# Kernel tuning notes

Hardware: AMD Instinct MI355X
Metric: run time of the kernel (lower is better)

## Reference

```python
import jax, jax.numpy as jnp
import numpy as np

N_NODES = 50000
N_EDGES = 800000
NODE_IN, EDGE_IN, EFT, OUT = 128, 64, 32, 64


def setup_inputs() -> dict:
    key = jax.random.key(0)
    ks = jax.random.split(key, 8)
    h = jax.random.normal(ks[0], (N_NODES, NODE_IN), dtype=jnp.float32)
    edge_feat = jax.random.normal(ks[1], (N_EDGES, EDGE_IN), dtype=jnp.float32)
    src = jax.random.randint(ks[2], (N_EDGES,), 0, N_NODES, dtype=jnp.int32)
    dst = jax.random.randint(ks[3], (N_EDGES,), 0, N_NODES, dtype=jnp.int32)
    Wn = jax.random.normal(ks[4], (OUT, NODE_IN), dtype=jnp.float32) * 0.05
    We = jax.random.normal(ks[5], (EFT, EDGE_IN), dtype=jnp.float32) * 0.05
    Wa = jax.random.normal(ks[6], (1, OUT + EFT + OUT), dtype=jnp.float32) * 0.05
    W2 = jax.random.normal(ks[7], (OUT, OUT + EFT), dtype=jnp.float32) * 0.05
    return {"h": h, "edge_feat": edge_feat, "src": src, "dst": dst,
            "Wn": Wn, "We": We, "Wa": Wa, "W2": W2}


def reference(h, edge_feat, src, dst, Wn, We, Wa, W2):
    N = h.shape[0]
    # node / edge feature projections (bias=False linears)
    z = h @ Wn.T                       # [N, OUT]
    ef = edge_feat @ We.T              # [E, EFT]
    # per-edge message: concat(src node ft, edge ft)
    zne = jnp.concatenate([z[src], ef], axis=1)            # [E, OUT+EFT]
    # attention logit: leaky_relu(attn_fc([zne, z_dst]))
    a = jnp.concatenate([zne, z[dst]], axis=1) @ Wa.T      # [E, 1]
    s = jax.nn.leaky_relu(a[:, 0], negative_slope=0.01)    # [E]
    # segment softmax over incoming edges of each dst node
    seg_max = jax.ops.segment_max(s, dst, num_segments=N)
    ex = jnp.exp(s - seg_max[dst])
    denom = jax.ops.segment_sum(ex, dst, num_segments=N)
    alpha = ex / denom[dst]                                # [E]
    # weighted scatter-sum aggregation, then fc2
    agg = jax.ops.segment_sum(alpha[:, None] * zne, dst, num_segments=N)
    h_new = agg @ W2.T                                     # [N, OUT]
    # DGL semantics: nodes with no incoming messages keep ndata['z'] = fc_n(h)
    deg = jax.ops.segment_sum(jnp.ones_like(s), dst, num_segments=N)
    return jnp.where((deg > 0)[:, None], h_new, z)
```

## Files before the change

kernel.cpp:

```cpp
#include <hip/hip_runtime.h>
#include <math.h>

#define N_NODES 50000
#define N_EDGES 800000
#define NB1 196

typedef __attribute__((ext_vector_type(8))) short bf16x8;
typedef __attribute__((ext_vector_type(4))) float f32x4;

__device__ __forceinline__ unsigned short f2bf(float f) {
    unsigned u = __float_as_uint(f);
    unsigned r = (u + 0x7FFFu + ((u >> 16) & 1u)) >> 16;
    return (unsigned short)r;
}
__device__ __forceinline__ float bf2f(unsigned short u) {
    return __uint_as_float(((unsigned)u) << 16);
}
__device__ __forceinline__ unsigned pack2bf(float a, float b) {
    return (unsigned)f2bf(a) | ((unsigned)f2bf(b) << 16);
}

__global__ __launch_bounds__(256) void kw_kernel(const float* __restrict__ We,
                                                 const float* __restrict__ Wa,
                                                 const float* __restrict__ Wn,
                                                 const float* __restrict__ W2,
                                                 short* __restrict__ Bpack,
                                                 int* __restrict__ degi) {
    int t = blockIdx.x * 256 + threadIdx.x;
    if (t < N_NODES) degi[t] = 0;
    if (t < 15360) {
        int f = t >> 9, u = t & 511, lane = u >> 3, j = u & 7;
        int c = lane & 15, G = lane >> 4;
        float v = 0.f;
        if (f < 4) {
            int s = f >> 1, n = f & 1;
            v = We[(16 * n + c) * 64 + 32 * s + 8 * G + j];
        } else if (f < 6) {
            int s = f - 4;
            if (c == 0) {
                int k = 32 * s + 8 * G + j;
                #pragma unroll
                for (int jj = 0; jj < 32; ++jj) v += Wa[64 + jj] * We[jj * 64 + k];
            }
        } else if (f < 22) {
            int qf = f - 6, s = qf >> 2, n = qf & 3;
            v = Wn[(16 * n + c) * 128 + 32 * s + 8 * G + j];
        } else {
            int qf = f - 22, s = qf >> 2, n = qf & 3;
            v = W2[(16 * n + c) * 96 + 32 * s + 8 * G + j];
        }
        Bpack[t] = (short)f2bf(v);
    }
}

__global__ __launch_bounds__(256) void node_hist_kernel(
    const float* __restrict__ h, const float* __restrict__ Wa,
    const short* __restrict__ Bpack, const int* __restrict__ dst,
    float* __restrict__ z, unsigned short* __restrict__ y16,
    float* __restrict__ asrc, float* __restrict__ adst,
    int* __restrict__ degi, int* __restrict__ ranks)
{
    __shared__ float zl[4][1088];
    int t = threadIdx.x;
    if (blockIdx.x >= 782) {
        int e = (blockIdx.x - 782) * 256 + t;
        if (e < N_EDGES) ranks[e] = atomicAdd(&degi[dst[e]], 1);
        return;
    }
    int w = t >> 6, l = t & 63, c = l & 15, G = l >> 4;
    int T = blockIdx.x * 4 + w;
    if (T >= 3125) return;
    int n0 = T * 16;
    const bf16x8* Bp = (const bf16x8*)Bpack;

    const float* hp = h + (size_t)(n0 + c) * 128 + 8 * G;
    bf16x8 a[4];
    #pragma unroll
    for (int s = 0; s < 4; ++s) {
        float4 lo = *(const float4*)(hp + 32 * s);
        float4 hi = *(const float4*)(hp + 32 * s + 4);
        a[s][0] = (short)f2bf(lo.x); a[s][1] = (short)f2bf(lo.y);
        a[s][2] = (short)f2bf(lo.z); a[s][3] = (short)f2bf(lo.w);
        a[s][4] = (short)f2bf(hi.x); a[s][5] = (short)f2bf(hi.y);
        a[s][6] = (short)f2bf(hi.z); a[s][7] = (short)f2bf(hi.w);
    }
    f32x4 acc[4] = {{0.f,0.f,0.f,0.f},{0.f,0.f,0.f,0.f},{0.f,0.f,0.f,0.f},{0.f,0.f,0.f,0.f}};
    #pragma unroll
    for (int n = 0; n < 4; ++n)
        #pragma unroll
        for (int s = 0; s < 4; ++s)
            acc[n] = __builtin_amdgcn_mfma_f32_16x16x32_bf16(a[s], Bp[(6 + 4*s + n)*64 + l], acc[n], 0, 0, 0);

    float was[4], wad[4];
    #pragma unroll
    for (int n = 0; n < 4; ++n) { was[n] = Wa[16*n + c]; wad[n] = Wa[96 + 16*n + c]; }

    #pragma unroll
    for (int r = 0; r < 4; ++r) {
        int row = n0 + 4 * G + r;
        #pragma unroll
        for (int n = 0; n < 4; ++n) {
            z[(size_t)row * 64 + 16 * n + c] = acc[n][r];
            zl[w][(4 * G + r) * 68 + 16 * n + c] = acc[n][r];
        }
        float ps = acc[0][r]*was[0] + acc[1][r]*was[1] + acc[2][r]*was[2] + acc[3][r]*was[3];
        float pd = acc[0][r]*wad[0] + acc[1][r]*wad[1] + acc[2][r]*wad[2] + acc[3][r]*wad[3];
        ps += __shfl_xor(ps, 1); ps += __shfl_xor(ps, 2);
        ps += __shfl_xor(ps, 4); ps += __shfl_xor(ps, 8);
        pd += __shfl_xor(pd, 1); pd += __shfl_xor(pd, 2);
        pd += __shfl_xor(pd, 4); pd += __shfl_xor(pd, 8);
        if (c == 0) { asrc[row] = ps; adst[row] = pd; }
    }

    bf16x8 ay[2];
    #pragma unroll
    for (int s = 0; s < 2; ++s)
        #pragma unroll
        for (int j = 0; j < 8; ++j)
            ay[s][j] = (short)f2bf(zl[w][c * 68 + 32 * s + 8 * G + j]);
    f32x4 accy[4] = {{0.f,0.f,0.f,0.f},{0.f,0.f,0.f,0.f},{0.f,0.f,0.f,0.f},{0.f,0.f,0.f,0.f}};
    #pragma unroll
    for (int n = 0; n < 4; ++n)
        #pragma unroll
        for (int s = 0; s < 2; ++s)
            accy[n] = __builtin_amdgcn_mfma_f32_16x16x32_bf16(ay[s], Bp[(22 + 4*s + n)*64 + l], accy[n], 0, 0, 0);
    #pragma unroll
    for (int r = 0; r < 4; ++r)
        #pragma unroll
        for (int n = 0; n < 4; ++n)
            y16[(size_t)(n0 + 4*G + r) * 64 + 16*n + c] = f2bf(accy[n][r]);
}

__global__ __launch_bounds__(256) void scan1_kernel(const int* __restrict__ degi,
                                                    int* __restrict__ partial) {
    int t = threadIdx.x, i = blockIdx.x * 256 + t;
    int d = (i < N_NODES) ? degi[i] : 0;
    #pragma unroll
    for (int off = 32; off; off >>= 1) d += __shfl_down(d, off);
    __shared__ int wsum[4];
    if ((t & 63) == 0) wsum[t >> 6] = d;
    __syncthreads();
    if (t == 0) partial[blockIdx.x] = wsum[0] + wsum[1] + wsum[2] + wsum[3];
}

__global__ __launch_bounds__(256) void scan2_kernel(int* __restrict__ partial) {
    __shared__ int s[256];
    int t = threadIdx.x;
    int v = (t < NB1) ? partial[t] : 0;
    s[t] = v; __syncthreads();
    for (int off = 1; off < 256; off <<= 1) {
        int x = (t >= off) ? s[t - off] : 0;
        __syncthreads();
        s[t] += x;
        __syncthreads();
    }
    if (t < NB1) partial[t] = s[t] - v;
}

__global__ __launch_bounds__(256) void scan3_kernel(const int* __restrict__ degi,
                                                    const int* __restrict__ partial,
                                                    int* __restrict__ start) {
    __shared__ int s[256];
    int t = threadIdx.x, i = blockIdx.x * 256 + t;
    int d = (i < N_NODES) ? degi[i] : 0;
    s[t] = d; __syncthreads();
    for (int off = 1; off < 256; off <<= 1) {
        int x = (t >= off) ? s[t - off] : 0;
        __syncthreads();
        s[t] += x;
        __syncthreads();
    }
    if (i < N_NODES) start[i] = partial[blockIdx.x] + s[t] - d;
}

__global__ __launch_bounds__(256, 2) void edge_scatter_kernel(
    const float* __restrict__ edge_feat, const int* __restrict__ src,
    const int* __restrict__ dst, const float* __restrict__ asrc,
    const float* __restrict__ adst, const short* __restrict__ Bpack,
    const int* __restrict__ ranks, const int* __restrict__ start,
    unsigned* __restrict__ gout, float* __restrict__ exarr,
    int2* __restrict__ edata)
{
    int t = threadIdx.x;
    if (blockIdx.x >= 3125) {
        int e = (blockIdx.x - 3125) * 256 + t;
        if (e < N_EDGES) edata[start[dst[e]] + ranks[e]] = make_int2(e, src[e]);
        return;
    }
    int w = t >> 6, l = t & 63;
    int c = l & 15, G = l >> 4;
    int wbase = blockIdx.x * 256 + w * 64;

    const bf16x8* Bp = (const bf16x8*)Bpack;
    bf16x8 b00 = Bp[0 * 64 + l];
    bf16x8 b01 = Bp[1 * 64 + l];
    bf16x8 b10 = Bp[2 * 64 + l];
    bf16x8 b11 = Bp[3 * 64 + l];
    bf16x8 b2a = Bp[4 * 64 + l];
    bf16x8 b2b = Bp[5 * 64 + l];

    int e = wbase + l;
    float apre = asrc[src[e]] + adst[dst[e]];
    float Ra[16];
    #pragma unroll
    for (int k = 0; k < 4; ++k)
        #pragma unroll
        for (int r = 0; r < 4; ++r)
            Ra[4 * k + r] = __shfl(apre, 16 * k + 4 * G + r);

    const float* efr = edge_feat + (size_t)(wbase + c) * 64 + G * 8;
    float4 n0 = *(const float4*)(efr);
    float4 n1 = *(const float4*)(efr + 4);
    float4 n2 = *(const float4*)(efr + 32);
    float4 n3 = *(const float4*)(efr + 36);

    #pragma unroll
    for (int k = 0; k < 4; ++k) {
        float4 c0 = n0, c1 = n1, c2 = n2, c3 = n3;
        if (k < 3) {
            const float* efn = edge_feat + (size_t)(wbase + 16 * (k + 1) + c) * 64 + G * 8;
            n0 = *(const float4*)(efn);
            n1 = *(const float4*)(efn + 4);
            n2 = *(const float4*)(efn + 32);
            n3 = *(const float4*)(efn + 36);
        }
        bf16x8 a0, a1;
        a0[0] = (short)f2bf(c0.x); a0[1] = (short)f2bf(c0.y);
        a0[2] = (short)f2bf(c0.z); a0[3] = (short)f2bf(c0.w);
        a0[4] = (short)f2bf(c1.x); a0[5] = (short)f2bf(c1.y);
        a0[6] = (short)f2bf(c1.z); a0[7] = (short)f2bf(c1.w);
        a1[0] = (short)f2bf(c2.x); a1[1] = (short)f2bf(c2.y);
        a1[2] = (short)f2bf(c2.z); a1[3] = (short)f2bf(c2.w);
        a1[4] = (short)f2bf(c3.x); a1[5] = (short)f2bf(c3.y);
        a1[6] = (short)f2bf(c3.z); a1[7] = (short)f2bf(c3.w);

        f32x4 acc0 = {0.f, 0.f, 0.f, 0.f};
        f32x4 acc1 = {0.f, 0.f, 0.f, 0.f};
        f32x4 acc2 = {0.f, 0.f, 0.f, 0.f};
        acc0 = __builtin_amdgcn_mfma_f32_16x16x32_bf16(a0, b00, acc0, 0, 0, 0);
        acc0 = __builtin_amdgcn_mfma_f32_16x16x32_bf16(a1, b10, acc0, 0, 0, 0);
        acc1 = __builtin_amdgcn_mfma_f32_16x16x32_bf16(a0, b01, acc1, 0, 0, 0);
        acc1 = __builtin_amdgcn_mfma_f32_16x16x32_bf16(a1, b11, acc1, 0, 0, 0);
        acc2 = __builtin_amdgcn_mfma_f32_16x16x32_bf16(a0, b2a, acc2, 0, 0, 0);
        acc2 = __builtin_amdgcn_mfma_f32_16x16x32_bf16(a1, b2b, acc2, 0, 0, 0);

        #pragma unroll
        for (int r = 0; r < 4; ++r) {
            int eo = wbase + 16 * k + 4 * G + r;
            gout[(size_t)eo * 16 + c] = pack2bf(acc0[r], acc1[r]);
            if (c == 0) {
                float aa = Ra[4 * k + r] + acc2[r];
                float sg = aa > 0.f ? aa : 0.01f * aa;
                exarr[eo] = __expf(sg);
            }
        }
    }
}

__global__ __launch_bounds__(256) void agg_kernel(
    const unsigned* __restrict__ gout, const float* __restrict__ exarr,
    const int2* __restrict__ edata, const ushort4* __restrict__ y16v,
    const int* __restrict__ start, const int* __restrict__ degi,
    const float* __restrict__ z, const float* __restrict__ W2,
    float* __restrict__ out)
{
    __shared__ float stu[4][164];
    __shared__ float sW2b[64 * 36];
    int t = threadIdx.x, w = t >> 6, l = t & 63, g = l >> 4, q = l & 15;
    for (int idx = t; idx < 64 * 32; idx += 256)
        sW2b[(idx >> 5) * 36 + (idx & 31)] = W2[(idx >> 5) * 96 + 64 + (idx & 31)];
    __syncthreads();

    int d    = blockIdx.x * 4 + w;
    int base = __builtin_amdgcn_readfirstlane(start[d]);
    int deg  = __builtin_amdgcn_readfirstlane(degi[d]);
    float2 tg = make_float2(0.f, 0.f);
    float4 uy4 = make_float4(0.f, 0.f, 0.f, 0.f);
    float den = 0.f;

    for (int c0 = 0; c0 < deg; c0 += 64) {
        int cc = min(deg - c0, 64);
        int meid = 0, msrc = 0; float mex = 0.f;
        if (l < cc) {
            int2 md = edata[base + c0 + l];
            meid = md.x; msrc = md.y;
            mex = exarr[md.x];
        }
        for (int cI = 0; cI < cc; cI += 16) {
            int e0, e1, e2, e3, s0, s1, s2, s3;
            float x0, x1, x2, x3;
            #define PREP(P, EP, SP, XP)                                      \
                { int sl = cI + 4 * P + g; bool vv = sl < cc;               \
                  int slc = vv ? sl : 0;                                     \
                  EP = __shfl(meid, slc); SP = __shfl(msrc, slc);            \
                  float xx = __shfl(mex, slc); XP = vv ? xx : 0.f; }
            PREP(0, e0, s0, x0) PREP(1, e1, s1, x1)
            PREP(2, e2, s2, x2) PREP(3, e3, s3, x3)
            #undef PREP
            unsigned ga0 = gout[(size_t)e0 * 16 + q];
            unsigned ga1 = gout[(size_t)e1 * 16 + q];
            unsigned ga2 = gout[(size_t)e2 * 16 + q];
            unsigned ga3 = gout[(size_t)e3 * 16 + q];
            ushort4 ya0 = y16v[(size_t)s0 * 16 + q];
            ushort4 ya1 = y16v[(size_t)s1 * 16 + q];
            ushort4 ya2 = y16v[(size_t)s2 * 16 + q];
            ushort4 ya3 = y16v[(size_t)s3 * 16 + q];
            #define ACCP(XP, GA, YA)                                         \
                { tg.x += XP * bf2f((unsigned short)(GA & 0xffffu));         \
                  tg.y += XP * bf2f((unsigned short)(GA >> 16));             \
                  uy4.x += XP * bf2f(YA.x); uy4.y += XP * bf2f(YA.y);        \
                  uy4.z += XP * bf2f(YA.z); uy4.w += XP * bf2f(YA.w);        \
                  den += XP; }
            ACCP(x0, ga0, ya0) ACCP(x1, ga1, ya1)
            ACCP(x2, ga2, ya2) ACCP(x3, ga3, ya3)
            #undef ACCP
        }
    }

    tg.x += __shfl_xor(tg.x, 16); tg.x += __shfl_xor(tg.x, 32);
    tg.y += __shfl_xor(tg.y, 16); tg.y += __shfl_xor(tg.y, 32);
    uy4.x += __shfl_xor(uy4.x, 16); uy4.x += __shfl_xor(uy4.x, 32);
    uy4.y += __shfl_xor(uy4.y, 16); uy4.y += __shfl_xor(uy4.y, 32);
    uy4.z += __shfl_xor(uy4.z, 16); uy4.z += __shfl_xor(uy4.z, 32);
    uy4.w += __shfl_xor(uy4.w, 16); uy4.w += __shfl_xor(uy4.w, 32);
    den += __shfl_xor(den, 16); den += __shfl_xor(den, 32);

    if (l < 16) {
        *(float4*)&stu[w][64 + q * 4] = uy4;
        stu[w][128 + q] = tg.x;
        stu[w][144 + q] = tg.y;
    }

    if (deg > 0) {
        float r = 0.f;
        #pragma unroll
        for (int k = 0; k < 8; ++k) {
            float4 wv = *(const float4*)&sW2b[l * 36 + k * 4];
            float4 vv = *(const float4*)&stu[w][128 + k * 4];
            r += wv.x * vv.x + wv.y * vv.y + wv.z * vv.z + wv.w * vv.w;
        }
        out[(size_t)d * 64 + l] = (r + stu[w][64 + l]) / den;
    } else {
        out[(size_t)d * 64 + l] = z[(size_t)d * 64 + l];
    }
}

extern "C" void kernel_launch(void* const* d_in, const int* in_sizes, int n_in,
                              void* d_out, int out_size, void* d_ws, size_t ws_size,
                              hipStream_t stream) {
    const float* h         = (const float*)d_in[0];
    const float* edge_feat = (const float*)d_in[1];
    const int*   src       = (const int*)d_in[2];
    const int*   dst       = (const int*)d_in[3];
    const float* Wn        = (const float*)d_in[4];
    const float* We        = (const float*)d_in[5];
    const float* Wa        = (const float*)d_in[6];
    const float* W2        = (const float*)d_in[7];
    float* out = (float*)d_out;

    char* p = (char*)d_ws;
    unsigned*       gout   = (unsigned*)p;       p += (size_t)N_EDGES * 16 * 4;
    float*          z      = (float*)p;          p += (size_t)N_NODES * 64 * 4;
    unsigned short* y16    = (unsigned short*)p; p += (size_t)N_NODES * 64 * 2;
    int2*           edata  = (int2*)p;           p += (size_t)N_EDGES * 8;
    float*          exarr  = (float*)p;          p += (size_t)N_EDGES * 4;
    float*          asrc   = (float*)p;          p += (size_t)N_NODES * 4;
    float*          adst   = (float*)p;          p += (size_t)N_NODES * 4;
    int*            degi   = (int*)p;            p += (size_t)N_NODES * 4;
    int*            start  = (int*)p;            p += (size_t)N_NODES * 4;
    int*            ranks  = (int*)p;            p += (size_t)N_EDGES * 4;
    int*            partial= (int*)p;            p += (size_t)256 * 4;
    short*          Bpack  = (short*)p;          p += (size_t)15360 * 2;

    kw_kernel<<<NB1, 256, 0, stream>>>(We, Wa, Wn, W2, Bpack, degi);
    node_hist_kernel<<<782 + 3125, 256, 0, stream>>>(h, Wa, Bpack, dst, z, y16,
                                                     asrc, adst, degi, ranks);
    scan1_kernel<<<NB1, 256, 0, stream>>>(degi, partial);
    scan2_kernel<<<1, 256, 0, stream>>>(partial);
    scan3_kernel<<<NB1, 256, 0, stream>>>(degi, partial, start);
    edge_scatter_kernel<<<3125 + 3125, 256, 0, stream>>>(edge_feat, src, dst, asrc, adst,
                                                         Bpack, ranks, start,
                                                         gout, exarr, edata);
    agg_kernel<<<N_NODES / 4, 256, 0, stream>>>(gout, exarr, edata, (const ushort4*)y16,
                                                start, degi, z, W2, out);
}
```

Measured before the change: 178.2 us.

## Fold W2 into edge projection and scatter full messages into dst-sorted slots

Precomputes W2[:,64:96]·We as a packed 64x64 weight, so the edge kernel produces the final 64-wide W2-projected message (edge part plus gathered y of the source node) per edge. Each message goes straight into its CSR slot by destination, along with the exp logit. The aggregation kernel then only streams contiguous bf16 rows and does a weighted sum, with no indirect gathers, edata indirection or W2 epilogue. The cost is a larger per-edge intermediate (64 bf16 instead of 32) written with scattered stores, and more MFMA work per edge.

```diff
diff --git a/kernel.cpp b/kernel.cpp
--- a/kernel.cpp
+++ b/kernel.cpp
@@ -28,25 +28,28 @@
                                                  int* __restrict__ degi) {
     int t = blockIdx.x * 256 + threadIdx.x;
     if (t < N_NODES) degi[t] = 0;
-    if (t < 15360) {
+    if (t < 34 * 512) {
         int f = t >> 9, u = t & 511, lane = u >> 3, j = u & 7;
         int c = lane & 15, G = lane >> 4;
         float v = 0.f;
-        if (f < 4) {
-            int s = f >> 1, n = f & 1;
-            v = We[(16 * n + c) * 64 + 32 * s + 8 * G + j];
-        } else if (f < 6) {
-            int s = f - 4;
+        if (f < 8) {
+            int s = f >> 2, n = f & 3;
+            int kp = 32 * s + 8 * G + j;
+            #pragma unroll
+            for (int kk = 0; kk < 32; ++kk)
+                v += W2[(16 * n + c) * 96 + 64 + kk] * We[kk * 64 + kp];
+        } else if (f < 10) {
+            int s = f - 8;
             if (c == 0) {
-                int k = 32 * s + 8 * G + j;
+                int kp = 32 * s + 8 * G + j;
                 #pragma unroll
-                for (int jj = 0; jj < 32; ++jj) v += Wa[64 + jj] * We[jj * 64 + k];
+                for (int jj = 0; jj < 32; ++jj) v += Wa[64 + jj] * We[jj * 64 + kp];
             }
-        } else if (f < 22) {
-            int qf = f - 6, s = qf >> 2, n = qf & 3;
+        } else if (f < 26) {
+            int qf = f - 10, s = qf >> 2, n = qf & 3;
             v = Wn[(16 * n + c) * 128 + 32 * s + 8 * G + j];
         } else {
-            int qf = f - 22, s = qf >> 2, n = qf & 3;
+            int qf = f - 26, s = qf >> 2, n = qf & 3;
             v = W2[(16 * n + c) * 96 + 32 * s + 8 * G + j];
         }
         Bpack[t] = (short)f2bf(v);
@@ -56,7 +59,7 @@
 __global__ __launch_bounds__(256) void node_hist_kernel(
     const float* __restrict__ h, const float* __restrict__ Wa,
     const short* __restrict__ Bpack, const int* __restrict__ dst,
-    float* __restrict__ z, unsigned short* __restrict__ y16,
+    float* __restrict__ z, ushort4* __restrict__ y16p,
     float* __restrict__ asrc, float* __restrict__ adst,
     int* __restrict__ degi, int* __restrict__ ranks)
 {
@@ -89,7 +92,7 @@
     for (int n = 0; n < 4; ++n)
         #pragma unroll
         for (int s = 0; s < 4; ++s)
-            acc[n] = __builtin_amdgcn_mfma_f32_16x16x32_bf16(a[s], Bp[(6 + 4*s + n)*64 + l], acc[n], 0, 0, 0);
+            acc[n] = __builtin_amdgcn_mfma_f32_16x16x32_bf16(a[s], Bp[(10 + 4*s + n)*64 + l], acc[n], 0, 0, 0);
 
     float was[4], wad[4];
     #pragma unroll
@@ -123,12 +126,14 @@
     for (int n = 0; n < 4; ++n)
         #pragma unroll
         for (int s = 0; s < 2; ++s)
-            accy[n] = __builtin_amdgcn_mfma_f32_16x16x32_bf16(ay[s], Bp[(22 + 4*s + n)*64 + l], accy[n], 0, 0, 0);
-    #pragma unroll
-    for (int r = 0; r < 4; ++r)
-        #pragma unroll
-        for (int n = 0; n < 4; ++n)
-            y16[(size_t)(n0 + 4*G + r) * 64 + 16*n + c] = f2bf(accy[n][r]);
+            accy[n] = __builtin_amdgcn_mfma_f32_16x16x32_bf16(ay[s], Bp[(26 + 4*s + n)*64 + l], accy[n], 0, 0, 0);
+    #pragma unroll
+    for (int r = 0; r < 4; ++r) {
+        ushort4 yo;
+        yo.x = f2bf(accy[0][r]); yo.y = f2bf(accy[1][r]);
+        yo.z = f2bf(accy[2][r]); yo.w = f2bf(accy[3][r]);
+        y16p[(size_t)(n0 + 4 * G + r) * 16 + c] = yo;
+    }
 }
 
 __global__ __launch_bounds__(256) void scan1_kernel(const int* __restrict__ degi,
@@ -173,40 +178,30 @@
     if (i < N_NODES) start[i] = partial[blockIdx.x] + s[t] - d;
 }
 
-__global__ __launch_bounds__(256, 2) void edge_scatter_kernel(
+__global__ __launch_bounds__(256, 2) void edge_kernel(
     const float* __restrict__ edge_feat, const int* __restrict__ src,
-    const int* __restrict__ dst, const float* __restrict__ asrc,
+    const int* __restrict__ dst, const int* __restrict__ ranks,
+    const int* __restrict__ start, const float* __restrict__ asrc,
     const float* __restrict__ adst, const short* __restrict__ Bpack,
-    const int* __restrict__ ranks, const int* __restrict__ start,
-    unsigned* __restrict__ gout, float* __restrict__ exarr,
-    int2* __restrict__ edata)
+    const ushort4* __restrict__ y16p,
+    unsigned short* __restrict__ wout, float* __restrict__ exslot)
 {
-    int t = threadIdx.x;
-    if (blockIdx.x >= 3125) {
-        int e = (blockIdx.x - 3125) * 256 + t;
-        if (e < N_EDGES) edata[start[dst[e]] + ranks[e]] = make_int2(e, src[e]);
-        return;
-    }
-    int w = t >> 6, l = t & 63;
+    int t = threadIdx.x, w = t >> 6, l = t & 63;
     int c = l & 15, G = l >> 4;
     int wbase = blockIdx.x * 256 + w * 64;
 
     const bf16x8* Bp = (const bf16x8*)Bpack;
-    bf16x8 b00 = Bp[0 * 64 + l];
-    bf16x8 b01 = Bp[1 * 64 + l];
-    bf16x8 b10 = Bp[2 * 64 + l];
-    bf16x8 b11 = Bp[3 * 64 + l];
-    bf16x8 b2a = Bp[4 * 64 + l];
-    bf16x8 b2b = Bp[5 * 64 + l];
+    bf16x8 bc[8];
+    #pragma unroll
+    for (int f = 0; f < 8; ++f) bc[f] = Bp[f * 64 + l];
+    bf16x8 b2a = Bp[8 * 64 + l];
+    bf16x8 b2b = Bp[9 * 64 + l];
 
     int e = wbase + l;
-    float apre = asrc[src[e]] + adst[dst[e]];
-    float Ra[16];
-    #pragma unroll
-    for (int k = 0; k < 4; ++k)
-        #pragma unroll
-        for (int r = 0; r < 4; ++r)
-            Ra[4 * k + r] = __shfl(apre, 16 * k + 4 * G + r);
+    int se = src[e];
+    int de = dst[e];
+    int slot = start[de] + ranks[e];
+    float apre = asrc[se] + adst[de];
 
     const float* efr = edge_feat + (size_t)(wbase + c) * 64 + G * 8;
     float4 n0 = *(const float4*)(efr);
@@ -224,6 +219,18 @@
             n2 = *(const float4*)(efn + 32);
             n3 = *(const float4*)(efn + 36);
         }
+        int sr[4], sl4[4]; float ap[4];
+        #pragma unroll
+        for (int r = 0; r < 4; ++r) {
+            int si = 16 * k + 4 * G + r;
+            sr[r]  = __shfl(se, si);
+            sl4[r] = __shfl(slot, si);
+            ap[r]  = __shfl(apre, si);
+        }
+        ushort4 yv[4];
+        #pragma unroll
+        for (int r = 0; r < 4; ++r) yv[r] = y16p[(size_t)sr[r] * 16 + c];
+
         bf16x8 a0, a1;
         a0[0] = (short)f2bf(c0.x); a0[1] = (short)f2bf(c0.y);
         a0[2] = (short)f2bf(c0.z); a0[3] = (short)f2bf(c0.w);
@@ -234,115 +241,66 @@
         a1[4] = (short)f2bf(c3.x); a1[5] = (short)f2bf(c3.y);
         a1[6] = (short)f2bf(c3.z); a1[7] = (short)f2bf(c3.w);
 
-        f32x4 acc0 = {0.f, 0.f, 0.f, 0.f};
-        f32x4 acc1 = {0.f, 0.f, 0.f, 0.f};
+        f32x4 acc[4] = {{0.f,0.f,0.f,0.f},{0.f,0.f,0.f,0.f},{0.f,0.f,0.f,0.f},{0.f,0.f,0.f,0.f}};
         f32x4 acc2 = {0.f, 0.f, 0.f, 0.f};
-        acc0 = __builtin_amdgcn_mfma_f32_16x16x32_bf16(a0, b00, acc0, 0, 0, 0);
-        acc0 = __builtin_amdgcn_mfma_f32_16x16x32_bf16(a1, b10, acc0, 0, 0, 0);
-        acc1 = __builtin_amdgcn_mfma_f32_16x16x32_bf16(a0, b01, acc1, 0, 0, 0);
-        acc1 = __builtin_amdgcn_mfma_f32_16x16x32_bf16(a1, b11, acc1, 0, 0, 0);
+        #pragma unroll
+        for (int n = 0; n < 4; ++n) {
+            acc[n] = __builtin_amdgcn_mfma_f32_16x16x32_bf16(a0, bc[n], acc[n], 0, 0, 0);
+            acc[n] = __builtin_amdgcn_mfma_f32_16x16x32_bf16(a1, bc[4 + n], acc[n], 0, 0, 0);
+        }
         acc2 = __builtin_amdgcn_mfma_f32_16x16x32_bf16(a0, b2a, acc2, 0, 0, 0);
         acc2 = __builtin_amdgcn_mfma_f32_16x16x32_bf16(a1, b2b, acc2, 0, 0, 0);
 
         #pragma unroll
         for (int r = 0; r < 4; ++r) {
-            int eo = wbase + 16 * k + 4 * G + r;
-            gout[(size_t)eo * 16 + c] = pack2bf(acc0[r], acc1[r]);
+            float u0 = acc[0][r] + bf2f(yv[r].x);
+            float u1 = acc[1][r] + bf2f(yv[r].y);
+            float u2 = acc[2][r] + bf2f(yv[r].z);
+            float u3 = acc[3][r] + bf2f(yv[r].w);
+            uint2 o;
+            o.x = pack2bf(u0, u1);
+            o.y = pack2bf(u2, u3);
+            *(uint2*)&wout[(size_t)sl4[r] * 64 + 4 * c] = o;
             if (c == 0) {
-                float aa = Ra[4 * k + r] + acc2[r];
+                float aa = ap[r] + acc2[r];
                 float sg = aa > 0.f ? aa : 0.01f * aa;
-                exarr[eo] = __expf(sg);
+                exslot[sl4[r]] = __expf(sg);
             }
         }
     }
 }
 
 __global__ __launch_bounds__(256) void agg_kernel(
-    const unsigned* __restrict__ gout, const float* __restrict__ exarr,
-    const int2* __restrict__ edata, const ushort4* __restrict__ y16v,
+    const unsigned short* __restrict__ wout, const float* __restrict__ exslot,
     const int* __restrict__ start, const int* __restrict__ degi,
-    const float* __restrict__ z, const float* __restrict__ W2,
-    float* __restrict__ out)
+    const float* __restrict__ z, float* __restrict__ out)
 {
-    __shared__ float stu[4][164];
-    __shared__ float sW2b[64 * 36];
-    int t = threadIdx.x, w = t >> 6, l = t & 63, g = l >> 4, q = l & 15;
-    for (int idx = t; idx < 64 * 32; idx += 256)
-        sW2b[(idx >> 5) * 36 + (idx & 31)] = W2[(idx >> 5) * 96 + 64 + (idx & 31)];
-    __syncthreads();
-
+    int t = threadIdx.x, w = t >> 6, l = t & 63;
     int d    = blockIdx.x * 4 + w;
     int base = __builtin_amdgcn_readfirstlane(start[d]);
     int deg  = __builtin_amdgcn_readfirstlane(degi[d]);
-    float2 tg = make_float2(0.f, 0.f);
-    float4 uy4 = make_float4(0.f, 0.f, 0.f, 0.f);
-    float den = 0.f;
-
-    for (int c0 = 0; c0 < deg; c0 += 64) {
-        int cc = min(deg - c0, 64);
-        int meid = 0, msrc = 0; float mex = 0.f;
-        if (l < cc) {
-            int2 md = edata[base + c0 + l];
-            meid = md.x; msrc = md.y;
-            mex = exarr[md.x];
-        }
-        for (int cI = 0; cI < cc; cI += 16) {
-            int e0, e1, e2, e3, s0, s1, s2, s3;
-            float x0, x1, x2, x3;
-            #define PREP(P, EP, SP, XP)                                      \
-                { int sl = cI + 4 * P + g; bool vv = sl < cc;               \
-                  int slc = vv ? sl : 0;                                     \
-                  EP = __shfl(meid, slc); SP = __shfl(msrc, slc);            \
-                  float xx = __shfl(mex, slc); XP = vv ? xx : 0.f; }
-            PREP(0, e0, s0, x0) PREP(1, e1, s1, x1)
-            PREP(2, e2, s2, x2) PREP(3, e3, s3, x3)
-            #undef PREP
-            unsigned ga0 = gout[(size_t)e0 * 16 + q];
-            unsigned ga1 = gout[(size_t)e1 * 16 + q];
-            unsigned ga2 = gout[(size_t)e2 * 16 + q];
-            unsigned ga3 = gout[(size_t)e3 * 16 + q];
-            ushort4 ya0 = y16v[(size_t)s0 * 16 + q];
-            ushort4 ya1 = y16v[(size_t)s1 * 16 + q];
-            ushort4 ya2 = y16v[(size_t)s2 * 16 + q];
-            ushort4 ya3 = y16v[(size_t)s3 * 16 + q];
-            #define ACCP(XP, GA, YA)                                         \
-                { tg.x += XP * bf2f((unsigned short)(GA & 0xffffu));         \
-                  tg.y += XP * bf2f((unsigned short)(GA >> 16));             \
-                  uy4.x += XP * bf2f(YA.x); uy4.y += XP * bf2f(YA.y);        \
-                  uy4.z += XP * bf2f(YA.z); uy4.w += XP * bf2f(YA.w);        \
-                  den += XP; }
-            ACCP(x0, ga0, ya0) ACCP(x1, ga1, ya1)
-            ACCP(x2, ga2, ya2) ACCP(x3, ga3, ya3)
-            #undef ACCP
-        }
-    }
-
-    tg.x += __shfl_xor(tg.x, 16); tg.x += __shfl_xor(tg.x, 32);
-    tg.y += __shfl_xor(tg.y, 16); tg.y += __shfl_xor(tg.y, 32);
-    uy4.x += __shfl_xor(uy4.x, 16); uy4.x += __shfl_xor(uy4.x, 32);
-    uy4.y += __shfl_xor(uy4.y, 16); uy4.y += __shfl_xor(uy4.y, 32);
-    uy4.z += __shfl_xor(uy4.z, 16); uy4.z += __shfl_xor(uy4.z, 32);
-    uy4.w += __shfl_xor(uy4.w, 16); uy4.w += __shfl_xor(uy4.w, 32);
-    den += __shfl_xor(den, 16); den += __shfl_xor(den, 32);
-
-    if (l < 16) {
-        *(float4*)&stu[w][64 + q * 4] = uy4;
-        stu[w][128 + q] = tg.x;
-        stu[w][144 + q] = tg.y;
-    }
-
-    if (deg > 0) {
-        float r = 0.f;
-        #pragma unroll
-        for (int k = 0; k < 8; ++k) {
-            float4 wv = *(const float4*)&sW2b[l * 36 + k * 4];
-            float4 vv = *(const float4*)&stu[w][128 + k * 4];
-            r += wv.x * vv.x + wv.y * vv.y + wv.z * vv.z + wv.w * vv.w;
-        }
-        out[(size_t)d * 64 + l] = (r + stu[w][64 + l]) / den;
-    } else {
-        out[(size_t)d * 64 + l] = z[(size_t)d * 64 + l];
-    }
+    const unsigned short* wp = wout + (size_t)base * 64 + l;
+    const float* xp = exslot + base;
+
+    float acc = 0.f, den = 0.f;
+    for (int i = 0; i < deg; i += 8) {
+        #pragma unroll
+        for (int j = 0; j < 8; ++j) {
+            int idx = i + j;
+            bool vld = idx < deg;
+            int ic = vld ? idx : deg - 1;
+            unsigned short v = wp[(size_t)ic * 64];
+            float x = vld ? xp[ic] : 0.f;
+            acc += x * bf2f(v);
+            den += x;
+        }
+    }
+
+    int comp = 16 * (l & 3) + (l >> 2);
+    if (deg > 0)
+        out[(size_t)d * 64 + comp] = acc / den;
+    else
+        out[(size_t)d * 64 + comp] = z[(size_t)d * 64 + comp];
 }
 
 extern "C" void kernel_launch(void* const* d_in, const int* in_sizes, int n_in,
@@ -359,28 +317,25 @@
     float* out = (float*)d_out;
 
     char* p = (char*)d_ws;
-    unsigned*       gout   = (unsigned*)p;       p += (size_t)N_EDGES * 16 * 4;
+    unsigned short* wout   = (unsigned short*)p; p += (size_t)N_EDGES * 64 * 2;
     float*          z      = (float*)p;          p += (size_t)N_NODES * 64 * 4;
-    unsigned short* y16    = (unsigned short*)p; p += (size_t)N_NODES * 64 * 2;
-    int2*           edata  = (int2*)p;           p += (size_t)N_EDGES * 8;
-    float*          exarr  = (float*)p;          p += (size_t)N_EDGES * 4;
+    ushort4*        y16p   = (ushort4*)p;        p += (size_t)N_NODES * 64 * 2;
+    float*          exslot = (float*)p;          p += (size_t)N_EDGES * 4;
     float*          asrc   = (float*)p;          p += (size_t)N_NODES * 4;
     float*          adst   = (float*)p;          p += (size_t)N_NODES * 4;
     int*            degi   = (int*)p;            p += (size_t)N_NODES * 4;
     int*            start  = (int*)p;            p += (size_t)N_NODES * 4;
     int*            ranks  = (int*)p;            p += (size_t)N_EDGES * 4;
     int*            partial= (int*)p;            p += (size_t)256 * 4;
-    short*          Bpack  = (short*)p;          p += (size_t)15360 * 2;
+    short*          Bpack  = (short*)p;          p += (size_t)34 * 512 * 2;
 
     kw_kernel<<<NB1, 256, 0, stream>>>(We, Wa, Wn, W2, Bpack, degi);
-    node_hist_kernel<<<782 + 3125, 256, 0, stream>>>(h, Wa, Bpack, dst, z, y16,
+    node_hist_kernel<<<782 + 3125, 256, 0, stream>>>(h, Wa, Bpack, dst, z, y16p,
                                                      asrc, adst, degi, ranks);
     scan1_kernel<<<NB1, 256, 0, stream>>>(degi, partial);
     scan2_kernel<<<1, 256, 0, stream>>>(partial);
     scan3_kernel<<<NB1, 256, 0, stream>>>(degi, partial, start);
-    edge_scatter_kernel<<<3125 + 3125, 256, 0, stream>>>(edge_feat, src, dst, asrc, adst,
-                                                         Bpack, ranks, start,
-                                                         gout, exarr, edata);
-    agg_kernel<<<N_NODES / 4, 256, 0, stream>>>(gout, exarr, edata, (const ushort4*)y16,
-                                                start, degi, z, W2, out);
-}
+    edge_kernel<<<3125, 256, 0, stream>>>(edge_feat, src, dst, ranks, start,
+                                          asrc, adst, Bpack, y16p, wout, exslot);
+    agg_kernel<<<N_NODES / 4, 256, 0, stream>>>(wout, exslot, start, degi, z, out);
+}
```

After: 169.2 us. 5.1% less time.
